# Performance work log

Measured on AMD Instinct MI355X. Metric: run time of the kernel, lower is better.

Reference implementation:

```python
import jax, jax.numpy as jnp
import numpy as np

N_VARS = 512
K = 32
B = 192
LOG2PI = 1.8378770664093453


def setup_inputs() -> dict:
    key = jax.random.key(0)
    k1, k2, k3, k4, k5 = jax.random.split(key, 5)
    X = jax.random.normal(k1, (B, N_VARS), dtype=jnp.float32)
    # one-hot cluster assignment matrix C: [n_vars, k]
    assign = jax.random.randint(k2, (N_VARS,), 0, K)
    C = jax.nn.one_hot(assign, K, dtype=jnp.float32)
    # cluster-level adjacency G: [k, k], binary
    G = (jax.random.uniform(k3, (K, K)) < 0.3).astype(jnp.float32)
    W = jax.random.normal(k4, (N_VARS, N_VARS), dtype=jnp.float32) / np.sqrt(N_VARS).astype(np.float32)
    b = jax.random.normal(k5, (N_VARS,), dtype=jnp.float32) * 0.01
    sigma = jnp.array([0.1], dtype=jnp.float32)
    rho = jnp.array([0.99], dtype=jnp.float32)
    return dict(X=X, C=C, G=G, W=W, b=b, sigma=sigma, rho=rho)


def reference(X, C, G, W, b, sigma, rho):
    n = X.shape[1]
    # expand cluster adjacency to variable-level mask: [n, n]
    G_expand = C @ G @ C.T
    # MaskedLinear: F.linear(X, W * mask, b)
    mean = X @ (W * G_expand).T + b  # [B, n]
    # cluster-structured covariance: sigma^2 * ((1-rho) I + rho * C C^T)
    M = C @ C.T  # same-cluster indicator (incl. diagonal)
    Cov = (sigma[0] ** 2) * ((1.0 - rho[0]) * jnp.eye(n, dtype=X.dtype) + rho[0] * M)
    L = jnp.linalg.cholesky(Cov)
    # torch MVN broadcasting: value [B,1,n] vs loc [B,n] -> log_prob [B,B]
    diff = X[:, None, :] - mean[None, :, :]  # [B, B, n]
    nb = diff.shape[0] * diff.shape[1]
    rhs = diff.reshape(nb, n).T  # [n, B*B]
    y = jax.scipy.linalg.solve_triangular(L, rhs, lower=True)  # [n, B*B]
    maha = jnp.sum(y * y, axis=0)  # [B*B]
    logdet = 2.0 * jnp.sum(jnp.log(jnp.diagonal(L)))
    logp = -0.5 * (maha + logdet + n * LOG2PI)
    return logp.mean()
```

## Files before the change

kernel.cpp:

```cpp
#include <hip/hip_runtime.h>
#include <math.h>

#define NV 512
#define KC 32
#define NB 192
#define LOG2PI 1.8378770664093453f

#define WS_COEF 512
#define WS_LOGDET 544
#define WS_XX 545
#define WS_MM 546
#define WS_SX1 548
#define WS_SX2 580
#define WS_U 676
#define WS_V 1188
#define WS_SM 1700
#define WS_TOTAL 7844

__global__ __launch_bounds__(256) void fused_kernel(
    const float* __restrict__ X, const float* __restrict__ C,
    const float* __restrict__ G, const float* __restrict__ W,
    const float* __restrict__ bias, const float* __restrict__ sigma,
    const float* __restrict__ rho, float* __restrict__ wsF, int* __restrict__ wsI)
{
    const int bid = blockIdx.x;
    const int tid = threadIdx.x;
    __shared__ int asg[NV];
    for (int n = tid; n < NV; n += 256) {
        const float* row = C + n * KC;
        int a = 0;
        #pragma unroll
        for (int c2 = 0; c2 < KC; ++c2) if (row[c2] > 0.5f) a = c2;
        asg[n] = a;
    }

    if (bid < 96) {
        __shared__ float Gs[KC * KC];
        __shared__ float Xs[32][33];
        __shared__ float Ws[32][33];
        __shared__ float vred[8][32];
        __shared__ float wred[4];
        for (int l = tid; l < KC * KC; l += 256) Gs[l] = G[l];
        __syncthreads();
        const int it = bid & 15, bt = bid >> 4;
        const int i0 = it * 32, b0 = bt * 32;
        const int tx = tid & 31, ty = tid >> 5;
        float acc[4] = {0.f, 0.f, 0.f, 0.f};
        for (int kt = 0; kt < 16; ++kt) {
            const int k0 = kt * 32;
            #pragma unroll
            for (int p = 0; p < 4; ++p) {
                const int l = tid + p * 256;
                const int rr = l >> 5, cc = l & 31;
                Xs[rr][cc] = X[(b0 + rr) * NV + k0 + cc];
                const int ir = i0 + rr;
                Ws[rr][cc] = W[ir * NV + k0 + cc] * Gs[asg[ir] * KC + asg[k0 + cc]];
            }
            __syncthreads();
            #pragma unroll
            for (int kk = 0; kk < 32; ++kk) {
                const float wv = Ws[tx][kk];
                #pragma unroll
                for (int r = 0; r < 4; ++r)
                    acc[r] += Xs[ty * 4 + r][kk] * wv;
            }
            __syncthreads();
        }
        const int i = i0 + tx;
        const float bi = bias[i];
        const int ci = asg[i];
        float* smG = wsF + WS_SM;
        float vpart = 0.f, mmpart = 0.f;
        #pragma unroll
        for (int r = 0; r < 4; ++r) {
            const float val = acc[r] + bi;
            vpart += val;
            mmpart += val * val;
            atomicAdd(&smG[(b0 + ty * 4 + r) * KC + ci], val);
        }
        vred[ty][tx] = vpart;
        for (int off = 32; off; off >>= 1) mmpart += __shfl_down(mmpart, off, 64);
        if ((tid & 63) == 0) wred[tid >> 6] = mmpart;
        __syncthreads();
        if (tid < 32) {
            float s = 0.f;
            #pragma unroll
            for (int q = 0; q < 8; ++q) s += vred[q][tid];
            atomicAdd(&wsF[WS_V + i0 + tid], s);
        }
        if (tid == 0) atomicAdd(&wsF[WS_MM], wred[0] + wred[1] + wred[2] + wred[3]);
    } else if (bid < 120) {
        __shared__ float smrow[KC];
        __shared__ float xred[4];
        __syncthreads();
        const int sb = bid - 96;
        const int c0 = tid * 2;
        const int ca = asg[c0], cb = asg[c0 + 1];
        float u0 = 0.f, u1 = 0.f, xxloc = 0.f, sx1acc = 0.f, sx2acc = 0.f;
        for (int r = 0; r < 8; ++r) {
            const int row = sb * 8 + r;
            if (tid < KC) smrow[tid] = 0.f;
            __syncthreads();
            const float2 xv = *(const float2*)(X + row * NV + c0);
            u0 += xv.x; u1 += xv.y;
            xxloc += xv.x * xv.x + xv.y * xv.y;
            atomicAdd(&smrow[ca], xv.x);
            atomicAdd(&smrow[cb], xv.y);
            __syncthreads();
            if (tid < KC) { const float s = smrow[tid]; sx1acc += s; sx2acc += s * s; }
            __syncthreads();
        }
        atomicAdd(&wsF[WS_U + c0], u0);
        atomicAdd(&wsF[WS_U + c0 + 1], u1);
        if (tid < KC) {
            atomicAdd(&wsF[WS_SX1 + tid], sx1acc);
            atomicAdd(&wsF[WS_SX2 + tid], sx2acc);
        }
        for (int off = 32; off; off >>= 1) xxloc += __shfl_down(xxloc, off, 64);
        if ((tid & 63) == 0) xred[tid >> 6] = xxloc;
        __syncthreads();
        if (tid == 0) atomicAdd(&wsF[WS_XX], xred[0] + xred[1] + xred[2] + xred[3]);
    } else {
        __shared__ int cnt[KC];
        __shared__ float ldred[KC];
        if (tid < KC) cnt[tid] = 0;
        __syncthreads();
        for (int n = tid; n < NV; n += 256) {
            atomicAdd(&cnt[asg[n]], 1);
            wsI[n] = asg[n];
        }
        __syncthreads();
        const float s2 = sigma[0] * sigma[0];
        const float rh = rho[0];
        const float av = s2 * (1.f - rh), bv = s2 * rh;
        if (tid < KC) {
            const int nc = cnt[tid];
            wsF[WS_COEF + tid] = bv / (av * (av + bv * (float)nc));
            ldred[tid] = (float)(nc - 1) * logf(av) + logf(av + bv * (float)nc);
        }
        __syncthreads();
        if (tid == 0) {
            float ld = 0.f;
            for (int c2 = 0; c2 < KC; ++c2) ld += ldred[c2];
            wsF[WS_LOGDET] = ld;
        }
    }
}

__global__ __launch_bounds__(256) void final_kernel(
    const float* __restrict__ sigma, const float* __restrict__ rho,
    const float* __restrict__ wsF, float* __restrict__ out)
{
    const int tid = threadIdx.x;
    __shared__ float SM1s[KC], SM2s[KC];
    __shared__ float red1[8][KC], red2[8][KC];
    __shared__ float crW[4];
    __shared__ float qsh;
    const float* sm = wsF + WS_SM;
    const int c = tid & 31, g = tid >> 5;
    float s1 = 0.f, s2sum = 0.f;
    for (int b = g; b < NB; b += 8) {
        const float s = sm[b * KC + c];
        s1 += s; s2sum += s * s;
    }
    red1[g][c] = s1; red2[g][c] = s2sum;
    __syncthreads();
    if (tid < KC) {
        float a1 = 0.f, a2 = 0.f;
        #pragma unroll
        for (int q = 0; q < 8; ++q) { a1 += red1[q][tid]; a2 += red2[q][tid]; }
        SM1s[tid] = a1; SM2s[tid] = a2;
    }
    __syncthreads();
    float cr = wsF[WS_U + tid] * wsF[WS_V + tid]
             + wsF[WS_U + 256 + tid] * wsF[WS_V + 256 + tid];
    for (int off = 32; off; off >>= 1) cr += __shfl_down(cr, off, 64);
    if ((tid & 63) == 0) crW[tid >> 6] = cr;
    float qv = 0.f;
    if (tid < KC) {
        const float coef = wsF[WS_COEF + tid];
        const float sx1 = wsF[WS_SX1 + tid], sx2 = wsF[WS_SX2 + tid];
        qv = coef * (sx2 * (1.f / NB) + SM2s[tid] * (1.f / NB)
                     - 2.f * sx1 * SM1s[tid] * (1.f / ((float)NB * (float)NB)));
    }
    for (int off = 16; off; off >>= 1) qv += __shfl_down(qv, off, 64);
    if (tid == 0) qsh = qv;
    __syncthreads();
    if (tid == 0) {
        const float crt = crW[0] + crW[1] + crW[2] + crW[3];
        const float s2 = sigma[0] * sigma[0];
        const float rh = rho[0];
        const float av = s2 * (1.f - rh);
        const float meanD2 = wsF[WS_XX] * (1.f / NB) + wsF[WS_MM] * (1.f / NB)
                           - 2.f * crt / ((float)NB * (float)NB);
        const float maha = meanD2 / av - qsh;
        out[0] = -0.5f * (maha + wsF[WS_LOGDET] + (float)NV * LOG2PI);
    }
}

extern "C" void kernel_launch(void* const* d_in, const int* in_sizes, int n_in,
                              void* d_out, int out_size, void* d_ws, size_t ws_size,
                              hipStream_t stream) {
    const float* X     = (const float*)d_in[0];
    const float* C     = (const float*)d_in[1];
    const float* G     = (const float*)d_in[2];
    const float* W     = (const float*)d_in[3];
    const float* b     = (const float*)d_in[4];
    const float* sigma = (const float*)d_in[5];
    const float* rho   = (const float*)d_in[6];
    float* wsF = (float*)d_ws;
    int*   wsI = (int*)d_ws;
    float* out = (float*)d_out;

    hipMemsetAsync(d_ws, 0, WS_TOTAL * sizeof(float), stream);
    hipLaunchKernelGGL(fused_kernel, dim3(121), dim3(256), 0, stream,
                       X, C, G, W, b, sigma, rho, wsF, wsI);
    hipLaunchKernelGGL(final_kernel, dim3(1), dim3(256), 0, stream,
                       sigma, rho, wsF, out);
}
```

Before: 97.34 us.

## Replace global atomics and memset with per-block partial slices reduced in finalize

Each block now writes its partial sums into a private workspace slice instead of doing global atomicAdds. This removes the need for the hipMemsetAsync, and the single finalize block sums across the slices. The GEMM tile switches to a transposed shared layout with 2x2 register blocking using float2 loads, and the stats blocks drop their per-row barriers by keeping 8 shared rows. The cost is a finalize kernel that reads more data from global memory.

```diff
diff --git a/kernel.cpp b/kernel.cpp
--- a/kernel.cpp
+++ b/kernel.cpp
@@ -6,195 +6,206 @@
 #define NB 192
 #define LOG2PI 1.8378770664093453f
 
-#define WS_COEF 512
-#define WS_LOGDET 544
-#define WS_XX 545
-#define WS_MM 546
-#define WS_SX1 548
-#define WS_SX2 580
-#define WS_U 676
-#define WS_V 1188
-#define WS_SM 1700
-#define WS_TOTAL 7844
-
-__global__ __launch_bounds__(256) void fused_kernel(
+#define WS_G 0
+#define G_STRIDE 1088
+#define WS_S 104448
+#define S_STRIDE 608
+#define WS_P 119040
+
+__global__ __launch_bounds__(256) void partial_kernel(
     const float* __restrict__ X, const float* __restrict__ C,
     const float* __restrict__ G, const float* __restrict__ W,
     const float* __restrict__ bias, const float* __restrict__ sigma,
-    const float* __restrict__ rho, float* __restrict__ wsF, int* __restrict__ wsI)
+    const float* __restrict__ rho, float* __restrict__ wsF)
 {
-    const int bid = blockIdx.x;
-    const int tid = threadIdx.x;
+    const int bid = blockIdx.x, tid = threadIdx.x;
     __shared__ int asg[NV];
+    __shared__ float Gs[KC * KC];
+    __shared__ float XsT[32][34];
+    __shared__ float WsT[32][34];
+    __shared__ float smtile[32 * KC];
+    __shared__ float varr[32];
+    __shared__ float redw[8];
+    __shared__ float smrows[8][KC];
+
     for (int n = tid; n < NV; n += 256) {
         const float* row = C + n * KC;
-        int a = 0;
-        #pragma unroll
-        for (int c2 = 0; c2 < KC; ++c2) if (row[c2] > 0.5f) a = c2;
-        asg[n] = a;
+        float a = 0.f;
+        #pragma unroll
+        for (int c = 0; c < KC; ++c) a += row[c] * (float)c;
+        asg[n] = (int)(a + 0.5f);
     }
 
     if (bid < 96) {
-        __shared__ float Gs[KC * KC];
-        __shared__ float Xs[32][33];
-        __shared__ float Ws[32][33];
-        __shared__ float vred[8][32];
-        __shared__ float wred[4];
         for (int l = tid; l < KC * KC; l += 256) Gs[l] = G[l];
-        __syncthreads();
-        const int it = bid & 15, bt = bid >> 4;
-        const int i0 = it * 32, b0 = bt * 32;
-        const int tx = tid & 31, ty = tid >> 5;
-        float acc[4] = {0.f, 0.f, 0.f, 0.f};
+        for (int l = tid; l < 32 * KC; l += 256) smtile[l] = 0.f;
+        if (tid < 32) varr[tid] = 0.f;
+        if (tid < 8) redw[tid] = 0.f;
+        __syncthreads();
+        const int i0 = (bid & 15) * 32, b0 = (bid >> 4) * 32;
+        const int tx = tid & 15, ty = tid >> 4;
+        float a00 = 0.f, a01 = 0.f, a10 = 0.f, a11 = 0.f;
         for (int kt = 0; kt < 16; ++kt) {
             const int k0 = kt * 32;
             #pragma unroll
             for (int p = 0; p < 4; ++p) {
                 const int l = tid + p * 256;
-                const int rr = l >> 5, cc = l & 31;
-                Xs[rr][cc] = X[(b0 + rr) * NV + k0 + cc];
-                const int ir = i0 + rr;
-                Ws[rr][cc] = W[ir * NV + k0 + cc] * Gs[asg[ir] * KC + asg[k0 + cc]];
+                const int r2 = l >> 5, c2 = l & 31;
+                XsT[c2][r2] = X[(b0 + r2) * NV + k0 + c2];
+                WsT[c2][r2] = W[(i0 + r2) * NV + k0 + c2]
+                            * Gs[asg[i0 + r2] * KC + asg[k0 + c2]];
             }
             __syncthreads();
             #pragma unroll
             for (int kk = 0; kk < 32; ++kk) {
-                const float wv = Ws[tx][kk];
-                #pragma unroll
-                for (int r = 0; r < 4; ++r)
-                    acc[r] += Xs[ty * 4 + r][kk] * wv;
+                const float2 xv = *(const float2*)&XsT[kk][ty * 2];
+                const float2 wv = *(const float2*)&WsT[kk][tx * 2];
+                a00 += xv.x * wv.x; a01 += xv.x * wv.y;
+                a10 += xv.y * wv.x; a11 += xv.y * wv.y;
             }
             __syncthreads();
         }
-        const int i = i0 + tx;
-        const float bi = bias[i];
-        const int ci = asg[i];
-        float* smG = wsF + WS_SM;
-        float vpart = 0.f, mmpart = 0.f;
-        #pragma unroll
-        for (int r = 0; r < 4; ++r) {
-            const float val = acc[r] + bi;
-            vpart += val;
-            mmpart += val * val;
-            atomicAdd(&smG[(b0 + ty * 4 + r) * KC + ci], val);
-        }
-        vred[ty][tx] = vpart;
-        for (int off = 32; off; off >>= 1) mmpart += __shfl_down(mmpart, off, 64);
-        if ((tid & 63) == 0) wred[tid >> 6] = mmpart;
-        __syncthreads();
-        if (tid < 32) {
-            float s = 0.f;
-            #pragma unroll
-            for (int q = 0; q < 8; ++q) s += vred[q][tid];
-            atomicAdd(&wsF[WS_V + i0 + tid], s);
-        }
-        if (tid == 0) atomicAdd(&wsF[WS_MM], wred[0] + wred[1] + wred[2] + wred[3]);
+        const int col0 = i0 + tx * 2, col1 = col0 + 1;
+        const float bf0 = bias[col0], bf1 = bias[col1];
+        const int ci0 = asg[col0], ci1 = asg[col1];
+        const int r0 = ty * 2, r1 = r0 + 1;
+        const float v00 = a00 + bf0, v01 = a01 + bf1;
+        const float v10 = a10 + bf0, v11 = a11 + bf1;
+        float mml = v00 * v00 + v01 * v01 + v10 * v10 + v11 * v11;
+        atomicAdd(&smtile[r0 * KC + ci0], v00);
+        atomicAdd(&smtile[r0 * KC + ci1], v01);
+        atomicAdd(&smtile[r1 * KC + ci0], v10);
+        atomicAdd(&smtile[r1 * KC + ci1], v11);
+        atomicAdd(&varr[tx * 2], v00 + v10);
+        atomicAdd(&varr[tx * 2 + 1], v01 + v11);
+        for (int off = 32; off; off >>= 1) mml += __shfl_down(mml, off, 64);
+        if ((tid & 63) == 0) redw[tid >> 6] = mml;
+        __syncthreads();
+        float* slice = wsF + WS_G + bid * G_STRIDE;
+        for (int l = tid; l < 32 * KC; l += 256) slice[l] = smtile[l];
+        if (tid < 32) slice[1024 + tid] = varr[tid];
+        if (tid == 0) slice[1056] = redw[0] + redw[1] + redw[2] + redw[3];
     } else if (bid < 120) {
-        __shared__ float smrow[KC];
-        __shared__ float xred[4];
-        __syncthreads();
-        const int sb = bid - 96;
+        for (int l = tid; l < 8 * KC; l += 256) ((float*)smrows)[l] = 0.f;
+        if (tid < 8) redw[tid] = 0.f;
+        __syncthreads();
+        const int sb = bid - 96, row0 = sb * 8;
         const int c0 = tid * 2;
         const int ca = asg[c0], cb = asg[c0 + 1];
-        float u0 = 0.f, u1 = 0.f, xxloc = 0.f, sx1acc = 0.f, sx2acc = 0.f;
+        float u0 = 0.f, u1 = 0.f, xx = 0.f;
+        #pragma unroll
         for (int r = 0; r < 8; ++r) {
-            const int row = sb * 8 + r;
-            if (tid < KC) smrow[tid] = 0.f;
-            __syncthreads();
-            const float2 xv = *(const float2*)(X + row * NV + c0);
+            const float2 xv = *(const float2*)(X + (row0 + r) * NV + c0);
             u0 += xv.x; u1 += xv.y;
-            xxloc += xv.x * xv.x + xv.y * xv.y;
-            atomicAdd(&smrow[ca], xv.x);
-            atomicAdd(&smrow[cb], xv.y);
-            __syncthreads();
-            if (tid < KC) { const float s = smrow[tid]; sx1acc += s; sx2acc += s * s; }
-            __syncthreads();
-        }
-        atomicAdd(&wsF[WS_U + c0], u0);
-        atomicAdd(&wsF[WS_U + c0 + 1], u1);
+            xx += xv.x * xv.x + xv.y * xv.y;
+            atomicAdd(&smrows[r][ca], xv.x);
+            atomicAdd(&smrows[r][cb], xv.y);
+        }
+        for (int off = 32; off; off >>= 1) xx += __shfl_down(xx, off, 64);
+        if ((tid & 63) == 0) redw[tid >> 6] = xx;
+        __syncthreads();
+        float* slice = wsF + WS_S + sb * S_STRIDE;
+        slice[c0] = u0; slice[c0 + 1] = u1;
         if (tid < KC) {
-            atomicAdd(&wsF[WS_SX1 + tid], sx1acc);
-            atomicAdd(&wsF[WS_SX2 + tid], sx2acc);
-        }
-        for (int off = 32; off; off >>= 1) xxloc += __shfl_down(xxloc, off, 64);
-        if ((tid & 63) == 0) xred[tid >> 6] = xxloc;
-        __syncthreads();
-        if (tid == 0) atomicAdd(&wsF[WS_XX], xred[0] + xred[1] + xred[2] + xred[3]);
+            float s1 = 0.f, s2 = 0.f;
+            #pragma unroll
+            for (int r = 0; r < 8; ++r) { const float s = smrows[r][tid]; s1 += s; s2 += s * s; }
+            slice[512 + tid] = s1;
+            slice[544 + tid] = s2;
+        }
+        if (tid == 0) slice[576] = redw[0] + redw[1] + redw[2] + redw[3];
     } else {
         __shared__ int cnt[KC];
         __shared__ float ldred[KC];
         if (tid < KC) cnt[tid] = 0;
         __syncthreads();
-        for (int n = tid; n < NV; n += 256) {
-            atomicAdd(&cnt[asg[n]], 1);
-            wsI[n] = asg[n];
-        }
-        __syncthreads();
-        const float s2 = sigma[0] * sigma[0];
-        const float rh = rho[0];
-        const float av = s2 * (1.f - rh), bv = s2 * rh;
+        for (int n = tid; n < NV; n += 256) atomicAdd(&cnt[asg[n]], 1);
+        __syncthreads();
+        const float s2v = sigma[0] * sigma[0], rh = rho[0];
+        const float av = s2v * (1.f - rh), bv = s2v * rh;
         if (tid < KC) {
             const int nc = cnt[tid];
-            wsF[WS_COEF + tid] = bv / (av * (av + bv * (float)nc));
+            wsF[WS_P + tid] = bv / (av * (av + bv * (float)nc));
             ldred[tid] = (float)(nc - 1) * logf(av) + logf(av + bv * (float)nc);
         }
         __syncthreads();
         if (tid == 0) {
             float ld = 0.f;
-            for (int c2 = 0; c2 < KC; ++c2) ld += ldred[c2];
-            wsF[WS_LOGDET] = ld;
+            for (int c = 0; c < KC; ++c) ld += ldred[c];
+            wsF[WS_P + 32] = ld;
         }
     }
 }
 
-__global__ __launch_bounds__(256) void final_kernel(
+__global__ __launch_bounds__(512) void finalize_kernel(
     const float* __restrict__ sigma, const float* __restrict__ rho,
     const float* __restrict__ wsF, float* __restrict__ out)
 {
     const int tid = threadIdx.x;
     __shared__ float SM1s[KC], SM2s[KC];
-    __shared__ float red1[8][KC], red2[8][KC];
-    __shared__ float crW[4];
-    __shared__ float qsh;
-    const float* sm = wsF + WS_SM;
-    const int c = tid & 31, g = tid >> 5;
-    float s1 = 0.f, s2sum = 0.f;
-    for (int b = g; b < NB; b += 8) {
-        const float s = sm[b * KC + c];
-        s1 += s; s2sum += s * s;
-    }
-    red1[g][c] = s1; red2[g][c] = s2sum;
+    __shared__ float accs[4];
+    if (tid < KC) { SM1s[tid] = 0.f; SM2s[tid] = 0.f; }
+    if (tid < 4) accs[tid] = 0.f;
     __syncthreads();
-    if (tid < KC) {
-        float a1 = 0.f, a2 = 0.f;
-        #pragma unroll
-        for (int q = 0; q < 8; ++q) { a1 += red1[q][tid]; a2 += red2[q][tid]; }
-        SM1s[tid] = a1; SM2s[tid] = a2;
+    const float* gS = wsF + WS_G;
+    const float* sS = wsF + WS_S;
+    #pragma unroll
+    for (int w = 0; w < 12; ++w) {
+        const int o = tid + w * 512;
+        const int b = o >> 5, c = o & 31;
+        const float* p = gS + (b >> 5) * 16 * G_STRIDE + (b & 31) * KC + c;
+        float s = 0.f;
+        #pragma unroll
+        for (int it = 0; it < 16; ++it) s += p[it * G_STRIDE];
+        atomicAdd(&SM1s[c], s);
+        atomicAdd(&SM2s[c], s * s);
+    }
+    {
+        const int i = tid;
+        const int it = i >> 5;
+        float v = 0.f;
+        #pragma unroll
+        for (int bt = 0; bt < 6; ++bt) v += gS[(bt * 16 + it) * G_STRIDE + 1024 + (i & 31)];
+        float u = 0.f;
+        #pragma unroll
+        for (int sb = 0; sb < 24; ++sb) u += sS[sb * S_STRIDE + i];
+        float cr = u * v;
+        for (int off = 32; off; off >>= 1) cr += __shfl_down(cr, off, 64);
+        if ((tid & 63) == 0) atomicAdd(&accs[2], cr);
+    }
+    {
+        float mm = (tid < 96) ? gS[tid * G_STRIDE + 1056] : 0.f;
+        for (int off = 32; off; off >>= 1) mm += __shfl_down(mm, off, 64);
+        if ((tid & 63) == 0) atomicAdd(&accs[0], mm);
+    }
+    {
+        float xx = (tid < 24) ? sS[tid * S_STRIDE + 576] : 0.f;
+        for (int off = 32; off; off >>= 1) xx += __shfl_down(xx, off, 64);
+        if ((tid & 63) == 0) atomicAdd(&accs[1], xx);
     }
     __syncthreads();
-    float cr = wsF[WS_U + tid] * wsF[WS_V + tid]
-             + wsF[WS_U + 256 + tid] * wsF[WS_V + 256 + tid];
-    for (int off = 32; off; off >>= 1) cr += __shfl_down(cr, off, 64);
-    if ((tid & 63) == 0) crW[tid >> 6] = cr;
     float qv = 0.f;
     if (tid < KC) {
-        const float coef = wsF[WS_COEF + tid];
-        const float sx1 = wsF[WS_SX1 + tid], sx2 = wsF[WS_SX2 + tid];
-        qv = coef * (sx2 * (1.f / NB) + SM2s[tid] * (1.f / NB)
-                     - 2.f * sx1 * SM1s[tid] * (1.f / ((float)NB * (float)NB)));
+        float s1 = 0.f, s2 = 0.f;
+        #pragma unroll
+        for (int sb = 0; sb < 24; ++sb) {
+            s1 += sS[sb * S_STRIDE + 512 + tid];
+            s2 += sS[sb * S_STRIDE + 544 + tid];
+        }
+        const float coef = wsF[WS_P + tid];
+        qv = coef * (s2 * (1.f / NB) + SM2s[tid] * (1.f / NB)
+                     - 2.f * s1 * SM1s[tid] * (1.f / ((float)NB * (float)NB)));
     }
     for (int off = 16; off; off >>= 1) qv += __shfl_down(qv, off, 64);
-    if (tid == 0) qsh = qv;
+    if (tid == 0) atomicAdd(&accs[3], qv);
     __syncthreads();
     if (tid == 0) {
-        const float crt = crW[0] + crW[1] + crW[2] + crW[3];
-        const float s2 = sigma[0] * sigma[0];
-        const float rh = rho[0];
-        const float av = s2 * (1.f - rh);
-        const float meanD2 = wsF[WS_XX] * (1.f / NB) + wsF[WS_MM] * (1.f / NB)
-                           - 2.f * crt / ((float)NB * (float)NB);
-        const float maha = meanD2 / av - qsh;
-        out[0] = -0.5f * (maha + wsF[WS_LOGDET] + (float)NV * LOG2PI);
+        const float s2v = sigma[0] * sigma[0], rh = rho[0];
+        const float av = s2v * (1.f - rh);
+        const float meanD2 = accs[1] * (1.f / NB) + accs[0] * (1.f / NB)
+                           - 2.f * accs[2] / ((float)NB * (float)NB);
+        const float maha = meanD2 / av - accs[3];
+        out[0] = -0.5f * (maha + wsF[WS_P + 32] + (float)NV * LOG2PI);
     }
 }
 
@@ -209,12 +220,10 @@
     const float* sigma = (const float*)d_in[5];
     const float* rho   = (const float*)d_in[6];
     float* wsF = (float*)d_ws;
-    int*   wsI = (int*)d_ws;
     float* out = (float*)d_out;
 
-    hipMemsetAsync(d_ws, 0, WS_TOTAL * sizeof(float), stream);
-    hipLaunchKernelGGL(fused_kernel, dim3(121), dim3(256), 0, stream,
-                       X, C, G, W, b, sigma, rho, wsF, wsI);
-    hipLaunchKernelGGL(final_kernel, dim3(1), dim3(256), 0, stream,
+    hipLaunchKernelGGL(partial_kernel, dim3(121), dim3(256), 0, stream,
+                       X, C, G, W, b, sigma, rho, wsF);
+    hipLaunchKernelGGL(finalize_kernel, dim3(1), dim3(512), 0, stream,
                        sigma, rho, wsF, out);
 }
```

Measured after the change: 106.7 us. 1.1x slower.
